# Kernel optimization log

Hardware: AMD Instinct MI355X
Metric: run time of the kernel (lower is better)

The kernel has to match this reference:

```python
import jax, jax.numpy as jnp
import numpy as np

N = 50000      # nodes
E = 800000     # edges (avg degree 16)
DIN = 128      # input_dim
DH = 128       # hidden_dim
H = 8          # num_heads
DK = DH // H   # 16
TN = 8         # num_node_types
TE = 8         # num_edge_types
NB = 4         # num_bases


def setup_inputs() -> dict:
    key = jax.random.key(0)
    ks = jax.random.split(key, 20)
    inp = {}
    inp['node_feat'] = jax.random.normal(ks[0], (N, DIN), jnp.float32)
    inp['node_type'] = jax.random.randint(ks[1], (N,), 0, TN)
    inp['src'] = jax.random.randint(ks[2], (E,), 0, N)
    inp['dst'] = jax.random.randint(ks[3], (E,), 0, N)
    inp['edge_type'] = jax.random.randint(ks[4], (E,), 0, TE)
    s = 0.05
    for i, nm in enumerate(['k', 'q', 'v', 'a']):
        inp['w_comp_' + nm] = jax.random.normal(ks[5 + 2 * i], (TN, NB), jnp.float32) * s
        inp['w_basis_' + nm] = jax.random.normal(ks[6 + 2 * i], (NB, DIN * DH), jnp.float32) * s
    inp['relation_pri'] = jnp.ones((TE, H), jnp.float32)
    inp['relation_att'] = jax.random.uniform(ks[13], (TE, H, DK, DK), jnp.float32, -0.25, 0.25)
    inp['relation_msg'] = jax.random.uniform(ks[14], (TE, H, DK, DK), jnp.float32, -0.25, 0.25)
    inp['loop_weight'] = jax.random.uniform(ks[15], (DIN, DH), jnp.float32, -0.08, 0.08)
    inp['bias'] = jnp.zeros((DH,), jnp.float32)
    return inp


def _decomp(x, nt, w_comp, w_basis):
    # basis regularizer: per-node-type weight W[t] = sum_b w_comp[t,b] * basis[b]
    T = w_comp.shape[0]
    W = (w_comp @ w_basis).reshape(T, x.shape[-1], -1)   # [T, in, out]
    h_all = jnp.einsum('ni,tio->tno', x, W)              # [T, N, out]
    return h_all[nt, jnp.arange(x.shape[0])]             # gather per-node type


def reference(node_feat, node_type, src, dst, edge_type,
              w_comp_k, w_basis_k, w_comp_q, w_basis_q,
              w_comp_v, w_basis_v, w_comp_a, w_basis_a,
              relation_pri, relation_att, relation_msg, loop_weight, bias):
    n = node_feat.shape[0]
    scale = (DH / H) ** -0.5
    # node init: k/q/v projections (per-node-type basis transforms)
    k = _decomp(node_feat, node_type, w_comp_k, w_basis_k).reshape(n, H, DK)
    q = _decomp(node_feat, node_type, w_comp_q, w_basis_q).reshape(n, H, DK)
    v = _decomp(node_feat, node_type, w_comp_v, w_basis_v).reshape(n, H, DK)
    # edge init: HGT attention. kt = k[src] @ relation_att[etype], computed
    # per-type at node granularity then gathered (avoids [E,H,dk,dk] gather).
    kt = jnp.einsum('nhi,thij->tnhj', k, relation_att)[edge_type, src]   # [E,H,dk]
    e = (q[dst] * kt).sum(-1) * relation_pri[edge_type] * scale          # [E,H]
    # edge softmax over incoming edges of each dst node
    m = jax.ops.segment_max(e, dst, num_segments=n)
    ex = jnp.exp(e - m[dst])
    denom = jax.ops.segment_sum(ex, dst, num_segments=n)
    a = ex / denom[dst]                                                  # [E,H]
    # message: v[src] @ relation_msg[etype], weighted by attention, sum-reduce
    vt = jnp.einsum('nhi,thij->tnhj', v, relation_msg)[edge_type, src]   # [E,H,dk]
    agg = jax.ops.segment_sum(a[..., None] * vt, dst, num_segments=n)    # [N,H,dk]
    agg = agg.reshape(n, DH)
    # node update: a_transform + self loop + bias + relu (dropout=0, no BN)
    out = _decomp(agg, node_type, w_comp_a, w_basis_a)
    out = out + node_feat @ loop_weight + bias
    return jax.nn.relu(out)
```

## Files before the change

### kernel.cpp

```cpp
#include <hip/hip_runtime.h>
#include <hip/hip_bf16.h>
#include <stdint.h>

#define DIN 128
#define DHID 128
#define TN 8
#define TE 8
#define NBASE 4

typedef short s8v __attribute__((ext_vector_type(8)));
typedef float f4v __attribute__((ext_vector_type(4)));

static __device__ __forceinline__ float bf2f(__hip_bfloat16 x){ return __bfloat162float(x); }
static __device__ __forceinline__ float lo16f(uint32_t u){ return __builtin_bit_cast(float, u << 16); }
static __device__ __forceinline__ float hi16f(uint32_t u){ return __builtin_bit_cast(float, u & 0xFFFF0000u); }
static __device__ __forceinline__ uint16_t f2bfu(float x){ return __builtin_bit_cast(uint16_t, __float2bfloat16(x)); }
static __device__ __forceinline__ uint32_t packbf2(float lo, float hi){
    return (uint32_t)f2bfu(lo) | ((uint32_t)f2bfu(hi) << 16);
}
static __device__ __forceinline__ float ldf(const void* p, int i, int flag){
    return flag ? ((const float*)p)[i] : bf2f(((const __hip_bfloat16*)p)[i]);
}
template<int CTRL>
static __device__ __forceinline__ float dpp_add(float x){
    int xi = __builtin_bit_cast(int, x);
    int yi = __builtin_amdgcn_update_dpp(xi, xi, CTRL, 0xF, 0xF, true);
    return x + __builtin_bit_cast(float, yi);
}

__global__ void k_prep(const int* __restrict__ dst, const int* __restrict__ etv, int E,
                       const int* __restrict__ ntype, int Nn,
                       const void* __restrict__ xin,
                       const void* __restrict__ ck, const void* __restrict__ bk,
                       const void* __restrict__ cq, const void* __restrict__ bq,
                       const void* __restrict__ cv, const void* __restrict__ bv,
                       const void* __restrict__ ca, const void* __restrict__ ba,
                       const void* __restrict__ lw, const void* __restrict__ rpri,
                       const void* __restrict__ ratt, const void* __restrict__ rmsg,
                       int* __restrict__ deg8, int* __restrict__ tcount,
                       uint32_t* __restrict__ xbf,
                       __hip_bfloat16* __restrict__ WkqvT, __hip_bfloat16* __restrict__ WfinT,
                       uint32_t* __restrict__ Apk, uint32_t* __restrict__ Mpk,
                       int* __restrict__ dflag)
{
    int flag = (((const uint32_t*)rpri)[0] == 0x3F803F80u) ? 0 : 1;
    __shared__ int lt[TN];
    if (threadIdx.x < TN) lt[threadIdx.x] = 0;
    __syncthreads();
    int gid = blockIdx.x * 256 + threadIdx.x;
    int stride = gridDim.x * 256;
    if (gid == 0) dflag[0] = flag;
    const int NW = Nn * 64;
    const int T3 = TN * 3 * 128 * 128;
    const int T4 = TN * 128 * 256;
    for (int e = gid; e < E; e += stride)
        atomicAdd(&deg8[dst[e] * 8 + etv[e]], 1);
    for (int n = gid; n < Nn; n += stride)
        atomicAdd(&lt[ntype[n]], 1);
    if (flag) {
        const float2* f = (const float2*)xin;
        for (int w = gid; w < NW; w += stride) { float2 v = f[w]; xbf[w] = packbf2(v.x, v.y); }
    } else {
        const uint32_t* s = (const uint32_t*)xin;
        for (int w = gid; w < NW; w += stride) xbf[w] = s[w];
    }
    for (int idx = gid; idx < T3; idx += stride) {
        int t = idx / 49152; int r = idx % 49152;
        int proj = r / 16384; int r2 = r % 16384;
        int j = r2 >> 7; int i = r2 & 127;
        const void* c = (proj == 0) ? ck : ((proj == 1) ? cq : cv);
        const void* b = (proj == 0) ? bk : ((proj == 1) ? bq : bv);
        float s = 0.f;
        #pragma unroll
        for (int bb = 0; bb < NBASE; ++bb)
            s += ldf(c, t * NBASE + bb, flag) * ldf(b, bb * 16384 + i * 128 + j, flag);
        WkqvT[idx] = __float2bfloat16(s);
    }
    for (int r = gid; r < T4; r += stride) {
        int t = r >> 15; int r2 = r & 32767;
        int j = r2 >> 8; int kk = r2 & 255;
        float s;
        if (kk < 128) {
            s = 0.f;
            #pragma unroll
            for (int bb = 0; bb < NBASE; ++bb)
                s += ldf(ca, t * NBASE + bb, flag) * ldf(ba, bb * 16384 + kk * 128 + j, flag);
        } else {
            s = ldf(lw, (kk - 128) * 128 + j, flag);
        }
        WfinT[r] = __float2bfloat16(s);
    }
    for (int w = gid; w < 8192; w += stride) {
        int eh = w >> 7, blk = (w >> 3) & 15, p = w & 7;
        float ps = ldf(rpri, eh, flag) * 0.25f;
        float a0 = ldf(ratt, (eh * 16 + blk) * 16 + 2 * p, flag) * ps;
        float a1 = ldf(ratt, (eh * 16 + blk) * 16 + 2 * p + 1, flag) * ps;
        Apk[w] = packbf2(a0, a1);
        float m0 = ldf(rmsg, (eh * 16 + 2 * p) * 16 + blk, flag);
        float m1 = ldf(rmsg, (eh * 16 + 2 * p + 1) * 16 + blk, flag);
        Mpk[w] = packbf2(m0, m1);
    }
    __syncthreads();
    if (threadIdx.x < TN) atomicAdd(&tcount[threadIdx.x], lt[threadIdx.x]);
}

__global__ void __launch_bounds__(1024) k_scanA(const int* __restrict__ deg8, int n,
                                                int* __restrict__ bsum)
{
    __shared__ int ws[16];
    int i = blockIdx.x * 1024 + threadIdx.x;
    int v = (i < n) ? deg8[i] : 0;
    #pragma unroll
    for (int o = 1; o < 64; o <<= 1) v += __shfl_xor(v, o, 64);
    int lane = threadIdx.x & 63, wv = threadIdx.x >> 6;
    if (lane == 0) ws[wv] = v;
    __syncthreads();
    if (threadIdx.x == 0) {
        int s = 0;
        #pragma unroll
        for (int w = 0; w < 16; ++w) s += ws[w];
        bsum[blockIdx.x] = s;
    }
}

__global__ void __launch_bounds__(512) k_scanB(int* __restrict__ bsum, int nblk,
                                               const int* __restrict__ tcount,
                                               int* __restrict__ toff, int* __restrict__ tcur)
{
    __shared__ int ws[8];
    int t = threadIdx.x;
    int v = (t < nblk) ? bsum[t] : 0;
    int lane = t & 63, wv = t >> 6;
    int sc = v;
    #pragma unroll
    for (int o = 1; o < 64; o <<= 1) { int tt = __shfl_up(sc, o, 64); if (lane >= o) sc += tt; }
    if (lane == 63) ws[wv] = sc;
    __syncthreads();
    int wb = 0;
    for (int w = 0; w < wv; ++w) wb += ws[w];
    if (t < nblk) bsum[t] = wb + sc - v;
    if (t == 0) {
        int s = 0;
        for (int k = 0; k < TN; ++k) { toff[k] = s; tcur[k] = s; s += tcount[k]; }
        toff[TN] = s;
    }
}

__global__ void __launch_bounds__(1024) k_scanC(const int* __restrict__ deg8, int n,
                                                const int* __restrict__ bsum,
                                                int* __restrict__ eoff8, int* __restrict__ ecur8,
                                                int E)
{
    __shared__ int ws[16];
    int i = blockIdx.x * 1024 + threadIdx.x;
    int v = (i < n) ? deg8[i] : 0;
    int lane = threadIdx.x & 63, wv = threadIdx.x >> 6;
    int sc = v;
    #pragma unroll
    for (int o = 1; o < 64; o <<= 1) { int tt = __shfl_up(sc, o, 64); if (lane >= o) sc += tt; }
    if (lane == 63) ws[wv] = sc;
    __syncthreads();
    int wb = bsum[blockIdx.x];
    for (int w = 0; w < wv; ++w) wb += ws[w];
    int ex = wb + sc - v;
    if (i < n) { eoff8[i] = ex; ecur8[i] = ex; }
    if (i == 0) eoff8[n] = E;
}

__global__ void k_scatter(const int* __restrict__ src, const int* __restrict__ dst,
                          const int* __restrict__ etv, int E,
                          const int* __restrict__ ntype, int Nn,
                          int* __restrict__ ecur8, int* __restrict__ esrc,
                          int* __restrict__ tcur, int* __restrict__ perm)
{
    int stride = gridDim.x * blockDim.x;
    int i0 = blockIdx.x * blockDim.x + threadIdx.x;
    for (int e = i0; e < E; e += stride) {
        int p = atomicAdd(&ecur8[dst[e] * 8 + etv[e]], 1);
        esrc[p] = src[e];
    }
    for (int n = i0; n < Nn; n += stride) {
        int p = atomicAdd(&tcur[ntype[n]], 1);
        perm[p] = n;
    }
}

__global__ void __launch_bounds__(256, 1) k_proj(
    const __hip_bfloat16* __restrict__ xbf,
    const __hip_bfloat16* __restrict__ WkqvT,
    const int* __restrict__ perm, const int* __restrict__ ntype,
    __hip_bfloat16* __restrict__ k16, __hip_bfloat16* __restrict__ q16,
    __hip_bfloat16* __restrict__ v16, int Nn)
{
    int lane = threadIdx.x & 63;
    int wave = blockIdx.x * 4 + (threadIdx.x >> 6);
    int row0 = wave * 16;
    if (row0 >= Nn) return;
    int col = lane & 15, quad = lane >> 4;
    int ar = row0 + col;
    int anode = perm[(ar < Nn) ? ar : (Nn - 1)];
    int tfirst = ntype[perm[row0]];
    int last_i = row0 + 15; if (last_i >= Nn) last_i = Nn - 1;
    int tlast = ntype[perm[last_i]];
    int onode[4], otype[4];
    #pragma unroll
    for (int r = 0; r < 4; ++r) {
        int oi = row0 + quad * 4 + r;
        bool v = (oi < Nn);
        onode[r] = perm[v ? oi : (Nn - 1)];
        otype[r] = v ? ntype[onode[r]] : -1;
    }
    const s8v* arow = (const s8v*)(xbf + (size_t)anode * DIN);
    for (int t = tfirst; t <= tlast; ++t) {
        f4v acc[24];
        #pragma unroll
        for (int nb = 0; nb < 24; ++nb) acc[nb] = (f4v){0.f, 0.f, 0.f, 0.f};
        const __hip_bfloat16* bbase = WkqvT + (size_t)t * 49152;
        #pragma unroll
        for (int kq = 0; kq < 4; ++kq) {
            s8v a = arow[kq * 4 + quad];
            #pragma unroll
            for (int nb = 0; nb < 24; ++nb) {
                int J = nb * 16 + col;
                s8v b = *((const s8v*)(bbase + (size_t)J * 128) + (kq * 4 + quad));
                acc[nb] = __builtin_amdgcn_mfma_f32_16x16x32_bf16(a, b, acc[nb], 0, 0, 0);
            }
        }
        #pragma unroll
        for (int nb = 0; nb < 24; ++nb) {
            int jj = ((nb * 16) & 127) + col;
            __hip_bfloat16* outp = (nb < 8) ? k16 : ((nb < 16) ? q16 : v16);
            #pragma unroll
            for (int r = 0; r < 4; ++r) {
                if (otype[r] == t) outp[(size_t)onode[r] * DHID + jj] = __float2bfloat16(acc[nb][r]);
            }
        }
    }
}

__global__ void __launch_bounds__(256, 6) k_edge(
    const uint32_t* __restrict__ kp, const uint32_t* __restrict__ qp,
    const uint32_t* __restrict__ vp,
    const uint32_t* __restrict__ Apk, const uint32_t* __restrict__ Mpk,
    const int* __restrict__ eoff8, const int* __restrict__ esrc,
    uint32_t* __restrict__ agg, int Nn)
{
    __shared__ float sS[4][164];
    int tid = threadIdx.x;
    int lane = tid & 63;
    int wv = tid >> 6;
    int h = lane >> 3, x = lane & 7;
    float* Srow = &sS[wv][h * 20];
    int wid = blockIdx.x * 4 + wv;
    int nw = gridDim.x * 4;
    for (int n = wid; n < Nn; n += nw) {
        const uint4* qb = (const uint4*)(qp + (size_t)n * 64 + h * 8);
        uint4 qw0 = qb[0], qw1 = qb[1];
        uint32_t qarr[8] = {qw0.x, qw0.y, qw0.z, qw0.w, qw1.x, qw1.y, qw1.z, qw1.w};
        float qv[16];
        #pragma unroll
        for (int p = 0; p < 8; ++p) { qv[2 * p] = lo16f(qarr[p]); qv[2 * p + 1] = hi16f(qarr[p]); }
        float l = 0.f, T0 = 0.f, T1 = 0.f;
        int pb = n * 8;
        int pnext = eoff8[pb];
        #pragma unroll 1
        for (int et = 0; et < 8; ++et) {
            int p0 = pnext;
            pnext = eoff8[pb + et + 1];
            int p1 = pnext;
            if (p0 >= p1) continue;
            const uint4* Ab = (const uint4*)(Apk + (((et * 8 + h) * 16 + 2 * x) * 8));
            uint4 A0 = Ab[0], A1 = Ab[1], A2 = Ab[2], A3 = Ab[3];
            uint32_t aw[16] = {A0.x, A0.y, A0.z, A0.w, A1.x, A1.y, A1.z, A1.w,
                               A2.x, A2.y, A2.z, A2.w, A3.x, A3.y, A3.z, A3.w};
            float qA0 = 0.f, qA1 = 0.f;
            #pragma unroll
            for (int p = 0; p < 8; ++p) {
                qA0 = fmaf(lo16f(aw[p]), qv[2 * p], qA0);
                qA0 = fmaf(hi16f(aw[p]), qv[2 * p + 1], qA0);
                qA1 = fmaf(lo16f(aw[8 + p]), qv[2 * p], qA1);
                qA1 = fmaf(hi16f(aw[8 + p]), qv[2 * p + 1], qA1);
            }
            float S0 = 0.f, S1 = 0.f;
            int sn = esrc[p0];
            uint32_t kw = kp[(size_t)sn * 64 + lane];
            uint32_t vw = vp[(size_t)sn * 64 + lane];
            for (int p = p0; p < p1; ++p) {
                uint32_t kc = kw, vc = vw;
                if (p + 1 < p1) {
                    int sn2 = esrc[p + 1];
                    kw = kp[(size_t)sn2 * 64 + lane];
                    vw = vp[(size_t)sn2 * 64 + lane];
                }
                float ep = fmaf(hi16f(kc), qA1, lo16f(kc) * qA0);
                ep = dpp_add<0xB1>(ep);
                ep = dpp_add<0x4E>(ep);
                ep = dpp_add<0x141>(ep);
                float exv = __expf(ep);
                l += exv;
                S0 = fmaf(exv, lo16f(vc), S0);
                S1 = fmaf(exv, hi16f(vc), S1);
            }
            float2 st; st.x = S0; st.y = S1;
            *(float2*)&Srow[2 * x] = st;
            float4 sv0 = *(const float4*)&Srow[0];
            float4 sv1 = *(const float4*)&Srow[4];
            float4 sv2 = *(const float4*)&Srow[8];
            float4 sv3 = *(const float4*)&Srow[12];
            float Sv[16] = {sv0.x, sv0.y, sv0.z, sv0.w, sv1.x, sv1.y, sv1.z, sv1.w,
                            sv2.x, sv2.y, sv2.z, sv2.w, sv3.x, sv3.y, sv3.z, sv3.w};
            const uint4* Mb = (const uint4*)(Mpk + (((et * 8 + h) * 16 + 2 * x) * 8));
            uint4 M0 = Mb[0], M1 = Mb[1], M2 = Mb[2], M3 = Mb[3];
            uint32_t mw[16] = {M0.x, M0.y, M0.z, M0.w, M1.x, M1.y, M1.z, M1.w,
                               M2.x, M2.y, M2.z, M2.w, M3.x, M3.y, M3.z, M3.w};
            #pragma unroll
            for (int p = 0; p < 8; ++p) {
                T0 = fmaf(lo16f(mw[p]), Sv[2 * p], T0);
                T0 = fmaf(hi16f(mw[p]), Sv[2 * p + 1], T0);
                T1 = fmaf(lo16f(mw[8 + p]), Sv[2 * p], T1);
                T1 = fmaf(hi16f(mw[8 + p]), Sv[2 * p + 1], T1);
            }
        }
        float inv = (l > 0.f) ? (1.f / l) : 0.f;
        agg[(size_t)n * 64 + lane] = packbf2(T0 * inv, T1 * inv);
    }
}

__global__ void __launch_bounds__(256, 1) k_final(
    const __hip_bfloat16* __restrict__ xbf,
    const __hip_bfloat16* __restrict__ aggbf,
    const __hip_bfloat16* __restrict__ WfinT,
    const void* __restrict__ bias,
    const int* __restrict__ perm, const int* __restrict__ ntype,
    void* __restrict__ outv, int Nn, const int* __restrict__ dflag)
{
    int flag = dflag[0];
    int lane = threadIdx.x & 63;
    int wave = blockIdx.x * 4 + (threadIdx.x >> 6);
    int row0 = wave * 16;
    if (row0 >= Nn) return;
    int col = lane & 15, quad = lane >> 4;
    int ar = row0 + col;
    int anode = perm[(ar < Nn) ? ar : (Nn - 1)];
    int tfirst = ntype[perm[row0]];
    int last_i = row0 + 15; if (last_i >= Nn) last_i = Nn - 1;
    int tlast = ntype[perm[last_i]];
    int onode[4], otype[4];
    #pragma unroll
    for (int r = 0; r < 4; ++r) {
        int oi = row0 + quad * 4 + r;
        bool v = (oi < Nn);
        onode[r] = perm[v ? oi : (Nn - 1)];
        otype[r] = v ? ntype[onode[r]] : -1;
    }
    const s8v* arow0 = (const s8v*)(aggbf + (size_t)anode * DHID);
    const s8v* arow1 = (const s8v*)(xbf + (size_t)anode * DIN);
    for (int t = tfirst; t <= tlast; ++t) {
        f4v acc[8];
        #pragma unroll
        for (int nb = 0; nb < 8; ++nb) acc[nb] = (f4v){0.f, 0.f, 0.f, 0.f};
        const __hip_bfloat16* bbase = WfinT + (size_t)t * 32768;
        #pragma unroll
        for (int kq = 0; kq < 8; ++kq) {
            s8v a = (kq < 4) ? arow0[kq * 4 + quad] : arow1[(kq - 4) * 4 + quad];
            #pragma unroll
            for (int nb = 0; nb < 8; ++nb) {
                int J = nb * 16 + col;
                s8v b = *((const s8v*)(bbase + (size_t)J * 256) + (kq * 4 + quad));
                acc[nb] = __builtin_amdgcn_mfma_f32_16x16x32_bf16(a, b, acc[nb], 0, 0, 0);
            }
        }
        #pragma unroll
        for (int nb = 0; nb < 8; ++nb) {
            int J = nb * 16 + col;
            float bj = ldf(bias, J, flag);
            #pragma unroll
            for (int r = 0; r < 4; ++r) {
                if (otype[r] == t) {
                    float val = fmaxf(acc[nb][r] + bj, 0.f);
                    size_t oi = (size_t)onode[r] * DHID + J;
                    if (flag) ((float*)outv)[oi] = val;
                    else ((__hip_bfloat16*)outv)[oi] = __float2bfloat16(val);
                }
            }
        }
    }
}

extern "C" void kernel_launch(void* const* d_in, const int* in_sizes, int n_in,
                              void* d_out, int out_size, void* d_ws, size_t ws_size,
                              hipStream_t stream)
{
    const void* xfeat = d_in[0];
    const int* ntype = (const int*)d_in[1];
    const int* srcv  = (const int*)d_in[2];
    const int* dstv  = (const int*)d_in[3];
    const int* etypv = (const int*)d_in[4];
    const void* ck = d_in[5];
    const void* bk = d_in[6];
    const void* cq = d_in[7];
    const void* bq = d_in[8];
    const void* cv = d_in[9];
    const void* bv = d_in[10];
    const void* ca = d_in[11];
    const void* ba = d_in[12];
    const void* rpri = d_in[13];
    const void* ratt = d_in[14];
    const void* rmsg = d_in[15];
    const void* lw   = d_in[16];
    const void* bias = d_in[17];
    int Nn = in_sizes[1];
    int E  = in_sizes[2];

    char* w = (char*)d_ws;
    size_t off = 0;
    auto alloc = [&](size_t b) -> char* {
        char* r = w + off;
        off = (off + b + 255) & ~(size_t)255;
        return r;
    };
    __hip_bfloat16* WkqvT = (__hip_bfloat16*)alloc((size_t)TN * 3 * 128 * 128 * 2);
    __hip_bfloat16* WfinT = (__hip_bfloat16*)alloc((size_t)TN * 256 * 128 * 2);
    __hip_bfloat16* xbf = (__hip_bfloat16*)alloc((size_t)Nn * 128 * 2);
    __hip_bfloat16* k16 = (__hip_bfloat16*)alloc((size_t)Nn * 128 * 2);
    __hip_bfloat16* q16 = (__hip_bfloat16*)alloc((size_t)Nn * 128 * 2);
    __hip_bfloat16* v16 = (__hip_bfloat16*)alloc((size_t)Nn * 128 * 2);
    __hip_bfloat16* aggbf = (__hip_bfloat16*)alloc((size_t)Nn * 128 * 2);
    uint32_t* Apk = (uint32_t*)alloc(8192 * 4);
    uint32_t* Mpk = (uint32_t*)alloc(8192 * 4);
    int n8 = Nn * 8;
    int* deg8   = (int*)alloc((size_t)(n8 + TN) * 4);
    int* tcount = deg8 + n8;
    int* eoff8  = (int*)alloc((size_t)(n8 + 1) * 4);
    int* ecur8  = (int*)alloc((size_t)n8 * 4);
    int nblk = (n8 + 1023) / 1024;
    int* bsum   = (int*)alloc((size_t)(nblk + 8) * 4);
    int* toff   = (int*)alloc((TN + 1) * 4);
    int* tcur   = (int*)alloc(TN * 4);
    int* perm   = (int*)alloc((size_t)Nn * 4);
    int* esrc   = (int*)alloc((size_t)E * 4);
    int* dflag  = (int*)alloc(4);

    hipMemsetAsync(deg8, 0, (size_t)(n8 + TN) * 4, stream);
    k_prep<<<2048, 256, 0, stream>>>(dstv, etypv, E, ntype, Nn, xfeat,
                                     ck, bk, cq, bq, cv, bv, ca, ba, lw, rpri, ratt, rmsg,
                                     deg8, tcount, (uint32_t*)xbf, WkqvT, WfinT, Apk, Mpk, dflag);
    k_scanA<<<nblk, 1024, 0, stream>>>(deg8, n8, bsum);
    k_scanB<<<1, 512, 0, stream>>>(bsum, nblk, tcount, toff, tcur);
    k_scanC<<<nblk, 1024, 0, stream>>>(deg8, n8, bsum, eoff8, ecur8, E);
    k_scatter<<<2048, 256, 0, stream>>>(srcv, dstv, etypv, E, ntype, Nn, ecur8, esrc, tcur, perm);
    int tiles = (Nn + 15) / 16;
    int pblocks = (tiles + 3) / 4;
    k_proj<<<pblocks, 256, 0, stream>>>(xbf, WkqvT, perm, ntype, k16, q16, v16, Nn);
    k_edge<<<2048, 256, 0, stream>>>((const uint32_t*)k16, (const uint32_t*)q16,
                                     (const uint32_t*)v16, Apk, Mpk, eoff8, esrc,
                                     (uint32_t*)aggbf, Nn);
    k_final<<<pblocks, 256, 0, stream>>>(xbf, aggbf, WfinT, bias, perm, ntype,
                                         d_out, Nn, dflag);
}
```

Baseline: 754.7 us.

## Interleave K/V rows, deepen edge gather prefetch, and widen projection tiles to 32 rows

The separate K and V buffers are merged into one interleaved per-node row, so each source gather in the edge kernel reads K and V from adjacent memory. The edge loop now keeps a software prefetch queue four edges deep across edge types, plus source indices a further four ahead, instead of prefetching only the next edge, to hide gather latency. The projection and final kernels each process two 16-row tiles per wave so every weight fragment load feeds two MFMAs, and the projection runs K, Q and V as separate passes to limit register use. The deeper prefetch costs registers, so edge-kernel occupancy bounds drop, and the projection kernels raise their waves-per-EU hint.

```diff
diff --git a/kernel.cpp b/kernel.cpp
--- a/kernel.cpp
+++ b/kernel.cpp
@@ -21,6 +21,7 @@
 static __device__ __forceinline__ float ldf(const void* p, int i, int flag){
     return flag ? ((const float*)p)[i] : bf2f(((const __hip_bfloat16*)p)[i]);
 }
+static __device__ __forceinline__ int imin(int a, int b){ return a < b ? a : b; }
 template<int CTRL>
 static __device__ __forceinline__ float dpp_add(float x){
     int xi = __builtin_bit_cast(int, x);
@@ -185,75 +186,108 @@
     }
 }
 
-__global__ void __launch_bounds__(256, 1) k_proj(
+__global__ void __launch_bounds__(256, 2) k_proj(
     const __hip_bfloat16* __restrict__ xbf,
     const __hip_bfloat16* __restrict__ WkqvT,
     const int* __restrict__ perm, const int* __restrict__ ntype,
-    __hip_bfloat16* __restrict__ k16, __hip_bfloat16* __restrict__ q16,
-    __hip_bfloat16* __restrict__ v16, int Nn)
+    uint32_t* __restrict__ kv, __hip_bfloat16* __restrict__ q16, int Nn)
 {
     int lane = threadIdx.x & 63;
     int wave = blockIdx.x * 4 + (threadIdx.x >> 6);
-    int row0 = wave * 16;
+    int row0 = wave * 32;
     if (row0 >= Nn) return;
     int col = lane & 15, quad = lane >> 4;
-    int ar = row0 + col;
-    int anode = perm[(ar < Nn) ? ar : (Nn - 1)];
+    int anode[2], onode[2][4], otype[2][4];
+    #pragma unroll
+    for (int s = 0; s < 2; ++s) {
+        int r0 = row0 + s * 16;
+        int ar = r0 + col;
+        anode[s] = perm[(ar < Nn) ? ar : (Nn - 1)];
+        #pragma unroll
+        for (int r = 0; r < 4; ++r) {
+            int oi = r0 + quad * 4 + r;
+            bool v = (oi < Nn);
+            onode[s][r] = perm[v ? oi : (Nn - 1)];
+            otype[s][r] = v ? ntype[onode[s][r]] : -1;
+        }
+    }
     int tfirst = ntype[perm[row0]];
-    int last_i = row0 + 15; if (last_i >= Nn) last_i = Nn - 1;
-    int tlast = ntype[perm[last_i]];
-    int onode[4], otype[4];
-    #pragma unroll
-    for (int r = 0; r < 4; ++r) {
-        int oi = row0 + quad * 4 + r;
-        bool v = (oi < Nn);
-        onode[r] = perm[v ? oi : (Nn - 1)];
-        otype[r] = v ? ntype[onode[r]] : -1;
-    }
-    const s8v* arow = (const s8v*)(xbf + (size_t)anode * DIN);
+    int lastI = row0 + 31; if (lastI >= Nn) lastI = Nn - 1;
+    int tlast = ntype[perm[lastI]];
+    const s8v* arow0 = (const s8v*)(xbf + (size_t)anode[0] * DIN);
+    const s8v* arow1 = (const s8v*)(xbf + (size_t)anode[1] * DIN);
     for (int t = tfirst; t <= tlast; ++t) {
-        f4v acc[24];
-        #pragma unroll
-        for (int nb = 0; nb < 24; ++nb) acc[nb] = (f4v){0.f, 0.f, 0.f, 0.f};
-        const __hip_bfloat16* bbase = WkqvT + (size_t)t * 49152;
-        #pragma unroll
-        for (int kq = 0; kq < 4; ++kq) {
-            s8v a = arow[kq * 4 + quad];
-            #pragma unroll
-            for (int nb = 0; nb < 24; ++nb) {
-                int J = nb * 16 + col;
-                s8v b = *((const s8v*)(bbase + (size_t)J * 128) + (kq * 4 + quad));
-                acc[nb] = __builtin_amdgcn_mfma_f32_16x16x32_bf16(a, b, acc[nb], 0, 0, 0);
-            }
-        }
-        #pragma unroll
-        for (int nb = 0; nb < 24; ++nb) {
-            int jj = ((nb * 16) & 127) + col;
-            __hip_bfloat16* outp = (nb < 8) ? k16 : ((nb < 16) ? q16 : v16);
-            #pragma unroll
-            for (int r = 0; r < 4; ++r) {
-                if (otype[r] == t) outp[(size_t)onode[r] * DHID + jj] = __float2bfloat16(acc[nb][r]);
-            }
-        }
-    }
-}
-
-__global__ void __launch_bounds__(256, 6) k_edge(
-    const uint32_t* __restrict__ kp, const uint32_t* __restrict__ qp,
-    const uint32_t* __restrict__ vp,
+        #pragma unroll 1
+        for (int proj = 0; proj < 3; ++proj) {
+            f4v acc[2][8];
+            #pragma unroll
+            for (int s = 0; s < 2; ++s)
+                #pragma unroll
+                for (int nb = 0; nb < 8; ++nb) acc[s][nb] = (f4v){0.f, 0.f, 0.f, 0.f};
+            const __hip_bfloat16* bb = WkqvT + (size_t)t * 49152 + proj * 16384;
+            #pragma unroll
+            for (int kq = 0; kq < 4; ++kq) {
+                s8v a0 = arow0[kq * 4 + quad];
+                s8v a1 = arow1[kq * 4 + quad];
+                #pragma unroll
+                for (int nb = 0; nb < 8; ++nb) {
+                    int J = nb * 16 + col;
+                    s8v b = *((const s8v*)(bb + (size_t)J * 128) + (kq * 4 + quad));
+                    acc[0][nb] = __builtin_amdgcn_mfma_f32_16x16x32_bf16(a0, b, acc[0][nb], 0, 0, 0);
+                    acc[1][nb] = __builtin_amdgcn_mfma_f32_16x16x32_bf16(a1, b, acc[1][nb], 0, 0, 0);
+                }
+            }
+            #pragma unroll
+            for (int s = 0; s < 2; ++s)
+            #pragma unroll
+            for (int nb = 0; nb < 8; ++nb) {
+                int jj = nb * 16 + col;
+                #pragma unroll
+                for (int r = 0; r < 4; ++r) {
+                    if (otype[s][r] == t) {
+                        uint16_t hv = f2bfu(acc[s][nb][r]);
+                        size_t node = (size_t)onode[s][r];
+                        if (proj == 0)      ((uint16_t*)kv)[node * 256 + jj] = hv;
+                        else if (proj == 1) ((uint16_t*)q16)[node * 128 + jj] = hv;
+                        else                ((uint16_t*)kv)[node * 256 + 128 + jj] = hv;
+                    }
+                }
+            }
+        }
+    }
+}
+
+__global__ void __launch_bounds__(256, 4) k_edge(
+    const uint32_t* __restrict__ kvp, const uint32_t* __restrict__ qp,
     const uint32_t* __restrict__ Apk, const uint32_t* __restrict__ Mpk,
     const int* __restrict__ eoff8, const int* __restrict__ esrc,
     uint32_t* __restrict__ agg, int Nn)
 {
     __shared__ float sS[4][164];
-    int tid = threadIdx.x;
-    int lane = tid & 63;
-    int wv = tid >> 6;
+    int tid = threadIdx.x, lane = tid & 63, wv = tid >> 6;
     int h = lane >> 3, x = lane & 7;
     float* Srow = &sS[wv][h * 20];
     int wid = blockIdx.x * 4 + wv;
     int nw = gridDim.x * 4;
     for (int n = wid; n < Nn; n += nw) {
+        int pb = n * 8;
+        int P0 = eoff8[pb];
+        int P1 = eoff8[pb + 8];
+        if (P0 >= P1) { agg[(size_t)n * 64 + lane] = 0u; continue; }
+        int c1 = P1 - 1;
+        int s0 = esrc[P0];
+        int s1 = esrc[imin(P0 + 1, c1)];
+        int s2 = esrc[imin(P0 + 2, c1)];
+        int s3 = esrc[imin(P0 + 3, c1)];
+        uint32_t kb0 = kvp[(size_t)s0 * 128 + lane], vb0 = kvp[(size_t)s0 * 128 + 64 + lane];
+        uint32_t kb1 = kvp[(size_t)s1 * 128 + lane], vb1 = kvp[(size_t)s1 * 128 + 64 + lane];
+        uint32_t kb2 = kvp[(size_t)s2 * 128 + lane], vb2 = kvp[(size_t)s2 * 128 + 64 + lane];
+        uint32_t kb3 = kvp[(size_t)s3 * 128 + lane], vb3 = kvp[(size_t)s3 * 128 + 64 + lane];
+        int sn0 = esrc[imin(P0 + 4, c1)];
+        int sn1 = esrc[imin(P0 + 5, c1)];
+        int sn2 = esrc[imin(P0 + 6, c1)];
+        int sn3 = esrc[imin(P0 + 7, c1)];
+        int pk = P0 + 4, ps = P0 + 8;
         const uint4* qb = (const uint4*)(qp + (size_t)n * 64 + h * 8);
         uint4 qw0 = qb[0], qw1 = qb[1];
         uint32_t qarr[8] = {qw0.x, qw0.y, qw0.z, qw0.w, qw1.x, qw1.y, qw1.z, qw1.w};
@@ -261,14 +295,13 @@
         #pragma unroll
         for (int p = 0; p < 8; ++p) { qv[2 * p] = lo16f(qarr[p]); qv[2 * p + 1] = hi16f(qarr[p]); }
         float l = 0.f, T0 = 0.f, T1 = 0.f;
-        int pb = n * 8;
-        int pnext = eoff8[pb];
+        int pnext = P0;
         #pragma unroll 1
         for (int et = 0; et < 8; ++et) {
             int p0 = pnext;
             pnext = eoff8[pb + et + 1];
-            int p1 = pnext;
-            if (p0 >= p1) continue;
+            int p1r = pnext;
+            if (p0 >= p1r) continue;
             const uint4* Ab = (const uint4*)(Apk + (((et * 8 + h) * 16 + 2 * x) * 8));
             uint4 A0 = Ab[0], A1 = Ab[1], A2 = Ab[2], A3 = Ab[3];
             uint32_t aw[16] = {A0.x, A0.y, A0.z, A0.w, A1.x, A1.y, A1.z, A1.w,
@@ -282,16 +315,17 @@
                 qA1 = fmaf(hi16f(aw[8 + p]), qv[2 * p + 1], qA1);
             }
             float S0 = 0.f, S1 = 0.f;
-            int sn = esrc[p0];
-            uint32_t kw = kp[(size_t)sn * 64 + lane];
-            uint32_t vw = vp[(size_t)sn * 64 + lane];
-            for (int p = p0; p < p1; ++p) {
-                uint32_t kc = kw, vc = vw;
-                if (p + 1 < p1) {
-                    int sn2 = esrc[p + 1];
-                    kw = kp[(size_t)sn2 * 64 + lane];
-                    vw = vp[(size_t)sn2 * 64 + lane];
+            for (int p = p0; p < p1r; ++p) {
+                uint32_t kc = kb0, vc = vb0;
+                kb0 = kb1; vb0 = vb1; kb1 = kb2; vb1 = vb2; kb2 = kb3; vb2 = vb3;
+                if (pk < P1) {
+                    kb3 = kvp[(size_t)sn0 * 128 + lane];
+                    vb3 = kvp[(size_t)sn0 * 128 + 64 + lane];
                 }
+                ++pk;
+                sn0 = sn1; sn1 = sn2; sn2 = sn3;
+                sn3 = esrc[(ps < P1) ? ps : c1];
+                ++ps;
                 float ep = fmaf(hi16f(kc), qA1, lo16f(kc) * qA0);
                 ep = dpp_add<0xB1>(ep);
                 ep = dpp_add<0x4E>(ep);
@@ -326,7 +360,7 @@
     }
 }
 
-__global__ void __launch_bounds__(256, 1) k_final(
+__global__ void __launch_bounds__(256, 2) k_final(
     const __hip_bfloat16* __restrict__ xbf,
     const __hip_bfloat16* __restrict__ aggbf,
     const __hip_bfloat16* __restrict__ WfinT,
@@ -337,48 +371,60 @@
     int flag = dflag[0];
     int lane = threadIdx.x & 63;
     int wave = blockIdx.x * 4 + (threadIdx.x >> 6);
-    int row0 = wave * 16;
+    int row0 = wave * 32;
     if (row0 >= Nn) return;
     int col = lane & 15, quad = lane >> 4;
-    int ar = row0 + col;
-    int anode = perm[(ar < Nn) ? ar : (Nn - 1)];
+    int anode[2], onode[2][4], otype[2][4];
+    #pragma unroll
+    for (int s = 0; s < 2; ++s) {
+        int r0 = row0 + s * 16;
+        int ar = r0 + col;
+        anode[s] = perm[(ar < Nn) ? ar : (Nn - 1)];
+        #pragma unroll
+        for (int r = 0; r < 4; ++r) {
+            int oi = r0 + quad * 4 + r;
+            bool v = (oi < Nn);
+            onode[s][r] = perm[v ? oi : (Nn - 1)];
+            otype[s][r] = v ? ntype[onode[s][r]] : -1;
+        }
+    }
     int tfirst = ntype[perm[row0]];
-    int last_i = row0 + 15; if (last_i >= Nn) last_i = Nn - 1;
-    int tlast = ntype[perm[last_i]];
-    int onode[4], otype[4];
-    #pragma unroll
-    for (int r = 0; r < 4; ++r) {
-        int oi = row0 + quad * 4 + r;
-        bool v = (oi < Nn);
-        onode[r] = perm[v ? oi : (Nn - 1)];
-        otype[r] = v ? ntype[onode[r]] : -1;
-    }
-    const s8v* arow0 = (const s8v*)(aggbf + (size_t)anode * DHID);
-    const s8v* arow1 = (const s8v*)(xbf + (size_t)anode * DIN);
+    int lastI = row0 + 31; if (lastI >= Nn) lastI = Nn - 1;
+    int tlast = ntype[perm[lastI]];
+    const s8v* ag0 = (const s8v*)(aggbf + (size_t)anode[0] * DHID);
+    const s8v* ag1 = (const s8v*)(aggbf + (size_t)anode[1] * DHID);
+    const s8v* ax0 = (const s8v*)(xbf + (size_t)anode[0] * DIN);
+    const s8v* ax1 = (const s8v*)(xbf + (size_t)anode[1] * DIN);
     for (int t = tfirst; t <= tlast; ++t) {
-        f4v acc[8];
-        #pragma unroll
-        for (int nb = 0; nb < 8; ++nb) acc[nb] = (f4v){0.f, 0.f, 0.f, 0.f};
+        f4v acc[2][8];
+        #pragma unroll
+        for (int s = 0; s < 2; ++s)
+            #pragma unroll
+            for (int nb = 0; nb < 8; ++nb) acc[s][nb] = (f4v){0.f, 0.f, 0.f, 0.f};
         const __hip_bfloat16* bbase = WfinT + (size_t)t * 32768;
         #pragma unroll
         for (int kq = 0; kq < 8; ++kq) {
-            s8v a = (kq < 4) ? arow0[kq * 4 + quad] : arow1[(kq - 4) * 4 + quad];
+            s8v a0 = (kq < 4) ? ag0[kq * 4 + quad] : ax0[(kq - 4) * 4 + quad];
+            s8v a1 = (kq < 4) ? ag1[kq * 4 + quad] : ax1[(kq - 4) * 4 + quad];
             #pragma unroll
             for (int nb = 0; nb < 8; ++nb) {
                 int J = nb * 16 + col;
                 s8v b = *((const s8v*)(bbase + (size_t)J * 256) + (kq * 4 + quad));
-                acc[nb] = __builtin_amdgcn_mfma_f32_16x16x32_bf16(a, b, acc[nb], 0, 0, 0);
-            }
-        }
+                acc[0][nb] = __builtin_amdgcn_mfma_f32_16x16x32_bf16(a0, b, acc[0][nb], 0, 0, 0);
+                acc[1][nb] = __builtin_amdgcn_mfma_f32_16x16x32_bf16(a1, b, acc[1][nb], 0, 0, 0);
+            }
+        }
+        #pragma unroll
+        for (int s = 0; s < 2; ++s)
         #pragma unroll
         for (int nb = 0; nb < 8; ++nb) {
             int J = nb * 16 + col;
             float bj = ldf(bias, J, flag);
             #pragma unroll
             for (int r = 0; r < 4; ++r) {
-                if (otype[r] == t) {
-                    float val = fmaxf(acc[nb][r] + bj, 0.f);
-                    size_t oi = (size_t)onode[r] * DHID + J;
+                if (otype[s][r] == t) {
+                    float val = fmaxf(acc[s][nb][r] + bj, 0.f);
+                    size_t oi = (size_t)onode[s][r] * DHID + J;
                     if (flag) ((float*)outv)[oi] = val;
                     else ((__hip_bfloat16*)outv)[oi] = __float2bfloat16(val);
                 }
@@ -422,9 +468,8 @@
     __hip_bfloat16* WkqvT = (__hip_bfloat16*)alloc((size_t)TN * 3 * 128 * 128 * 2);
     __hip_bfloat16* WfinT = (__hip_bfloat16*)alloc((size_t)TN * 256 * 128 * 2);
     __hip_bfloat16* xbf = (__hip_bfloat16*)alloc((size_t)Nn * 128 * 2);
-    __hip_bfloat16* k16 = (__hip_bfloat16*)alloc((size_t)Nn * 128 * 2);
+    uint32_t* kv = (uint32_t*)alloc((size_t)Nn * 128 * 4);
     __hip_bfloat16* q16 = (__hip_bfloat16*)alloc((size_t)Nn * 128 * 2);
-    __hip_bfloat16* v16 = (__hip_bfloat16*)alloc((size_t)Nn * 128 * 2);
     __hip_bfloat16* aggbf = (__hip_bfloat16*)alloc((size_t)Nn * 128 * 2);
     uint32_t* Apk = (uint32_t*)alloc(8192 * 4);
     uint32_t* Mpk = (uint32_t*)alloc(8192 * 4);
@@ -449,11 +494,10 @@
     k_scanB<<<1, 512, 0, stream>>>(bsum, nblk, tcount, toff, tcur);
     k_scanC<<<nblk, 1024, 0, stream>>>(deg8, n8, bsum, eoff8, ecur8, E);
     k_scatter<<<2048, 256, 0, stream>>>(srcv, dstv, etypv, E, ntype, Nn, ecur8, esrc, tcur, perm);
-    int tiles = (Nn + 15) / 16;
-    int pblocks = (tiles + 3) / 4;
-    k_proj<<<pblocks, 256, 0, stream>>>(xbf, WkqvT, perm, ntype, k16, q16, v16, Nn);
-    k_edge<<<2048, 256, 0, stream>>>((const uint32_t*)k16, (const uint32_t*)q16,
-                                     (const uint32_t*)v16, Apk, Mpk, eoff8, esrc,
+    int stiles = (Nn + 31) / 32;
+    int pblocks = (stiles + 3) / 4;
+    k_proj<<<pblocks, 256, 0, stream>>>(xbf, WkqvT, perm, ntype, kv, q16, Nn);
+    k_edge<<<2048, 256, 0, stream>>>(kv, (const uint32_t*)q16, Apk, Mpk, eoff8, esrc,
                                      (uint32_t*)aggbf, Nn);
     k_final<<<pblocks, 256, 0, stream>>>(xbf, aggbf, WfinT, bias, perm, ntype,
                                          d_out, Nn, dflag);
```

Result: faster. 705.5 us (-6.5%).
